# Kernel tuning notes

Measured on AMD Instinct MI355X. Metric: run time of the kernel, lower is better.

Reference implementation:

```python
import jax, jax.numpy as jnp
import numpy as np

S, E, K, D = 50000, 20000, 128, 128  # students, exercises, knowledge, emb dim
NE = 800000                          # edges per polarity
B = 8192                             # batch of response logs
L = 3                                # gcn layers
TEMP, CONTROL = 0.2, 0.3


def setup_inputs() -> dict:
    key = jax.random.key(0)
    ks = jax.random.split(key, 40)

    def nrm(i, shape, scale=0.05):
        return jax.random.normal(ks[i], shape, jnp.float32) * scale

    def uni(i, shape):
        return jax.random.uniform(ks[i], shape, jnp.float32)

    inp = {
        'stu_id': jax.random.randint(ks[0], (B,), 0, S, jnp.int32),
        'exer_id': jax.random.randint(ks[1], (B,), 0, E, jnp.int32),
        'kn_emb': uni(2, (B, K)),
        'ui1_u': jax.random.randint(ks[3], (NE,), 0, S, jnp.int32),
        'ui1_i': jax.random.randint(ks[4], (NE,), 0, E, jnp.int32),
        'ui1_val': uni(5, (NE,)), 'iu1_val': uni(6, (NE,)),
        'eps_ui1': uni(7, (NE,)), 'eps_iu1': uni(8, (NE,)),
        'ui0_u': jax.random.randint(ks[9], (NE,), 0, S, jnp.int32),
        'ui0_i': jax.random.randint(ks[10], (NE,), 0, E, jnp.int32),
        'ui0_val': uni(11, (NE,)), 'iu0_val': uni(12, (NE,)),
        'eps_ui0': uni(13, (NE,)), 'eps_iu0': uni(14, (NE,)),
        # embeddings
        'student_emb': nrm(15, (S, D)), 'exercise_emb': nrm(16, (E, D)),
        'knowledge_emb': nrm(17, (K, D)),
        'stu_b': nrm(18, (S, 1)), 'exer_b': nrm(19, (E, 1)), 'disc': nrm(20, (E, 1)),
        # edge-gate MLPs (polarity 1 and 0)
        'W1_l1': nrm(21, (D, 2 * D)), 'b1_l1': jnp.zeros((D,), jnp.float32),
        'W2_l1': nrm(22, (1, D)), 'b2_l1': jnp.zeros((1,), jnp.float32),
        'W1_l0': nrm(23, (D, 2 * D)), 'b1_l0': jnp.zeros((D,), jnp.float32),
        'W2_l0': nrm(24, (1, D)), 'b2_l0': jnp.zeros((1,), jnp.float32),
        # PosLinear prednet
        'pw1': nrm(25, (256, K)), 'pb1': jnp.zeros((256,), jnp.float32),
        'pw2': nrm(26, (128, 256)), 'pb2': jnp.zeros((128,), jnp.float32),
        'pw3': nrm(27, (1, 128)), 'pb3': jnp.zeros((1,), jnp.float32),
    }
    return inp


def _gate(uids, iids, uemb, iemb, W1, b1, W2, b2, eps):
    # concrete-distribution edge gate; embeddings are detached in original code
    row = jax.lax.stop_gradient(uemb)[uids]          # [NE, D]
    col = jax.lax.stop_gradient(iemb)[iids]          # [NE, D]
    h = jax.nn.relu(jnp.concatenate([row, col], axis=1) @ W1.T + b1)
    logit = (h @ W2.T + b2).reshape(-1)              # [NE]
    eps = jnp.clip(eps, 1e-6, 1.0 - 1e-6)
    g = jnp.log(eps) - jnp.log1p(-eps)               # logistic noise
    return CONTROL * jax.nn.sigmoid((logit + g) / TEMP) + (1.0 - CONTROL)


def _spmm(rows, cols, vals, x, n_rows):
    # out[rows] += vals * x[cols]
    return jax.ops.segment_sum(vals[:, None] * x[cols], rows, num_segments=n_rows)


def _poslin(x, W, b):
    Wp = 2.0 * jax.nn.relu(-W) + W  # == |W|
    return x @ Wp.T + b


def reference(stu_id, exer_id, kn_emb, ui1_u, ui1_i, ui1_val, iu1_val, eps_ui1,
              eps_iu1, ui0_u, ui0_i, ui0_val, iu0_val, eps_ui0, eps_iu0,
              student_emb, exercise_emb, knowledge_emb, stu_b, exer_b, disc,
              W1_l1, b1_l1, W2_l1, b2_l1, W1_l0, b1_l0, W2_l0, b2_l0,
              pw1, pb1, pw2, pb2, pw3, pb3):
    # --- graph_learner: per-edge gates on all 4 sparse matrices ---
    v_ui1 = ui1_val * _gate(ui1_u, ui1_i, student_emb, exercise_emb, W1_l1, b1_l1, W2_l1, b2_l1, eps_ui1)
    v_iu1 = iu1_val * _gate(ui1_u, ui1_i, student_emb, exercise_emb, W1_l1, b1_l1, W2_l1, b2_l1, eps_iu1)
    v_ui0 = ui0_val * _gate(ui0_u, ui0_i, student_emb, exercise_emb, W1_l0, b1_l0, W2_l0, b2_l0, eps_ui0)
    v_iu0 = iu0_val * _gate(ui0_u, ui0_i, student_emb, exercise_emb, W1_l0, b1_l0, W2_l0, b2_l0, eps_iu0)

    # --- graph_representations: L rounds of sparse propagation, mean over layers ---
    stu, exer = student_emb, exercise_emb
    stu_sum, exer_sum = stu, exer
    for _ in range(L):
        u1 = _spmm(ui1_u, ui1_i, v_ui1, exer, S)
        i1 = _spmm(ui1_i, ui1_u, v_iu1, stu, E)
        u0 = _spmm(ui0_u, ui0_i, v_ui0, exer, S)
        i0 = _spmm(ui0_i, ui0_u, v_iu0, stu, E)
        stu, exer = u1 + u0, i1 + i0
        stu_sum = stu_sum + stu
        exer_sum = exer_sum + exer
    stu_final = stu_sum / (L + 1)
    exer_final = exer_sum / (L + 1)

    # --- NCDM-style prediction head with PosLinear MLP ---
    stat = jax.nn.sigmoid(stu_final[stu_id] @ knowledge_emb.T + stu_b[stu_id])   # [B, K]
    diff = jax.nn.sigmoid(exer_final[exer_id] @ knowledge_emb.T + exer_b[exer_id])
    e_d = jax.nn.sigmoid(disc[exer_id])                                          # [B, 1]
    x = e_d * (stat - diff) * kn_emb
    h = jax.nn.sigmoid(_poslin(x, pw1, pb1))
    h = jax.nn.sigmoid(_poslin(h, pw2, pb2))
    out = jax.nn.sigmoid(_poslin(h, pw3, pb3)).reshape(-1)                       # [B]
    return out
```

## Files before the change

### kernel.cpp

```cpp
#include <hip/hip_runtime.h>
#include <hip/hip_bf16.h>
#include <math.h>

#define S_N 50000
#define E_N 20000
#define K_N 128
#define D_N 128
#define NE_N 800000
#define B_N 8192
#define L_N 3
#define GATE_TILES (NE_N / 64)
#define NB_S 782
#define NB_E 313
#define BPAD 464
#define BSLACK 480

typedef __attribute__((ext_vector_type(4))) float floatx4;
typedef __attribute__((ext_vector_type(8))) short short8v;

__device__ __forceinline__ unsigned short f2bf(float x) {
  unsigned int u = __float_as_uint(x);
  u += 0x7FFFu + ((u >> 16) & 1u);
  return (unsigned short)(u >> 16);
}
__device__ __forceinline__ float bf2f(unsigned short u) {
  return __uint_as_float(((unsigned int)u) << 16);
}
__device__ __forceinline__ float sigm(float z) { return 1.0f / (1.0f + __expf(-z)); }

__device__ __forceinline__ unsigned char f2e4m3(float x) {
  unsigned int u = __float_as_uint(x);
  unsigned char s = (unsigned char)((u >> 24) & 0x80);
  int e = (int)((u >> 23) & 0xFF) - 127;
  unsigned int m = u & 0x7FFFFF;
  if (((u >> 23) & 0xFF) == 0) return s;
  if (e >= 9) return s | 0x7E;
  if (e < -10) return s;
  if (e >= -6) {
    unsigned int keep = m >> 20;
    unsigned int rest = m & 0xFFFFF;
    if (rest > 0x80000u || (rest == 0x80000u && (keep & 1))) keep++;
    if (keep == 8) { keep = 0; e++; if (e >= 9) return s | 0x7E; }
    unsigned char b = (unsigned char)(s | ((e + 7) << 3) | keep);
    if ((b & 0x7F) == 0x7F) b = s | 0x7E;
    return b;
  }
  int shift = -6 - e;
  unsigned int full = 0x800000u | m;
  unsigned int q = full >> (20 + shift);
  unsigned int rest = full & ((1u << (20 + shift)) - 1);
  unsigned int half = 1u << (19 + shift);
  if (rest > half || (rest == half && (q & 1))) q++;
  if (q == 8) return s | 0x08;
  return (unsigned char)(s | q);
}
__device__ __forceinline__ unsigned int pk4_fp8(float4 v) {
  return (unsigned int)f2e4m3(v.x) | ((unsigned int)f2e4m3(v.y) << 8) |
         ((unsigned int)f2e4m3(v.z) << 16) | ((unsigned int)f2e4m3(v.w) << 24);
}

__global__ void prep_kernel(const float* __restrict__ W1_l1, const float* __restrict__ W1_l0,
                            const float* __restrict__ pw1, const float* __restrict__ pw2,
                            const float* __restrict__ pw3, const float* __restrict__ ke,
                            unsigned int* __restrict__ w1f8_1, unsigned int* __restrict__ w1f8_0,
                            float* __restrict__ pw1T, float* __restrict__ pw2T,
                            float* __restrict__ pw3a, float* __restrict__ keT) {
  int i = blockIdx.x * blockDim.x + threadIdx.x;
  if (i < 8192) { w1f8_1[i] = pk4_fp8(((const float4*)W1_l1)[i]); return; }
  i -= 8192;
  if (i < 8192) { w1f8_0[i] = pk4_fp8(((const float4*)W1_l0)[i]); return; }
  i -= 8192;
  if (i < 32768) { int d = i >> 8, j = i & 255; pw1T[i] = fabsf(pw1[j * 128 + d]); return; }
  i -= 32768;
  if (i < 32768) { int d = i >> 7, j = i & 127; pw2T[i] = fabsf(pw2[j * 256 + d]); return; }
  i -= 32768;
  if (i < 128) { pw3a[i] = fabsf(pw3[i]); return; }
  i -= 128;
  if (i < 16384) { int d = i >> 7, k = i & 127; keT[i] = ke[k * 128 + d]; return; }
}

__global__ void init_bf_kernel(const float* __restrict__ se, const float* __restrict__ ee,
                               unsigned short* __restrict__ sbf, unsigned short* __restrict__ ebf,
                               unsigned int* __restrict__ sf8, unsigned int* __restrict__ ef8) {
  int i = blockIdx.x * blockDim.x + threadIdx.x;
  const int nS4 = S_N * 32, nE4 = E_N * 32;
  if (i < nS4) {
    float4 v = ((const float4*)se)[i];
    unsigned int lo = (unsigned int)f2bf(v.x) | ((unsigned int)f2bf(v.y) << 16);
    unsigned int hi = (unsigned int)f2bf(v.z) | ((unsigned int)f2bf(v.w) << 16);
    ((uint2*)sbf)[i] = make_uint2(lo, hi);
    sf8[i] = pk4_fp8(v);
    return;
  }
  i -= nS4;
  if (i < nE4) {
    float4 v = ((const float4*)ee)[i];
    unsigned int lo = (unsigned int)f2bf(v.x) | ((unsigned int)f2bf(v.y) << 16);
    unsigned int hi = (unsigned int)f2bf(v.z) | ((unsigned int)f2bf(v.w) << 16);
    ((uint2*)ebf)[i] = make_uint2(lo, hi);
    ef8[i] = pk4_fp8(v);
  }
}

__global__ void zero_kernel(int* __restrict__ p, int n) {
  int i = blockIdx.x * blockDim.x + threadIdx.x;
  if (i < n) p[i] = 0;
}

__global__ __launch_bounds__(256)
void histB_kernel(const int* __restrict__ u1, const int* __restrict__ i1,
                  const int* __restrict__ u0, const int* __restrict__ i0,
                  int* __restrict__ gHistS, int* __restrict__ gHistE) {
  __shared__ int hS[NB_S], hE[NB_E];
  int t = threadIdx.x;
  for (int b = t; b < NB_S; b += 256) hS[b] = 0;
  for (int b = t; b < NB_E; b += 256) hE[b] = 0;
  __syncthreads();
  int e0 = blockIdx.x * 2048;
  for (int k = 0; k < 8; ++k) {
    int e = e0 + k * 256 + t;
    if (e < NE_N) {
      atomicAdd(&hS[u1[e] >> 6], 1);
      atomicAdd(&hS[u0[e] >> 6], 1);
      atomicAdd(&hE[i1[e] >> 6], 1);
      atomicAdd(&hE[i0[e] >> 6], 1);
    }
  }
  __syncthreads();
  for (int b = t; b < NB_S; b += 256) if (hS[b]) atomicAdd(&gHistS[b], hS[b]);
  for (int b = t; b < NB_E; b += 256) if (hE[b]) atomicAdd(&gHistE[b], hE[b]);
}

__global__ __launch_bounds__(128)
void scanB_kernel(const int* __restrict__ gHistS, int* __restrict__ baseS,
                  int* __restrict__ gCurS, int* __restrict__ basePS,
                  const int* __restrict__ gHistE, int* __restrict__ baseE,
                  int* __restrict__ gCurE, int* __restrict__ basePE) {
  int w = threadIdx.x >> 6, l = threadIdx.x & 63;
  int n = w ? NB_E : NB_S;
  const int* src = w ? gHistE : gHistS;
  int* bs  = w ? baseE  : baseS;
  int* cur = w ? gCurE  : gCurS;
  int* bsP = w ? basePE : basePS;
  int carry = 0, carryP = 0;
  for (int base = 0; base < n; base += 64) {
    int i = base + l;
    int v = (i < n) ? src[i] : 0;
    int p = (i < n) ? ((v + BPAD + 15) & ~15) : 0;
    int x = v, y = p;
#pragma unroll
    for (int o = 1; o < 64; o <<= 1) {
      int xx = __shfl_up(x, o, 64);
      int yy = __shfl_up(y, o, 64);
      if (l >= o) { x += xx; y += yy; }
    }
    if (i < n) {
      int ex = carry + x - v;
      bs[i] = ex; cur[i] = ex;
      bsP[i] = carryP + y - p;
    }
    carry += __shfl(x, 63, 64);
    carryP += __shfl(y, 63, 64);
  }
  if (l == 0) { bs[n] = carry; bsP[n] = carryP; }
}

__global__ __launch_bounds__(512, 2)
void gate_kernel(const int* __restrict__ eu1, const int* __restrict__ ei1,
                 const int* __restrict__ eu0, const int* __restrict__ ei0,
                 const unsigned char* __restrict__ sf8, const unsigned char* __restrict__ ef8,
                 const unsigned char* __restrict__ w1f8_1, const unsigned char* __restrict__ w1f8_0,
                 const float* __restrict__ b1_1, const float* __restrict__ w2_1,
                 const float* __restrict__ b2_1,
                 const float* __restrict__ b1_0, const float* __restrict__ w2_0,
                 const float* __restrict__ b2_0,
                 float* __restrict__ logit1, float* __restrict__ logit0) {
  __shared__ unsigned char Xl[2][64 * 272];
  __shared__ float plds[8][16];
  const int* eu; const int* ei; const unsigned char* w1f8;
  const float *b1p, *w2p, *b2p; float* lg;
  if (blockIdx.x < 2048) {
    eu = eu1; ei = ei1; w1f8 = w1f8_1; b1p = b1_1; w2p = w2_1; b2p = b2_1; lg = logit1;
  } else {
    eu = eu0; ei = ei0; w1f8 = w1f8_0; b1p = b1_0; w2p = w2_0; b2p = b2_0; lg = logit0;
  }
  int bb = blockIdx.x & 2047;
  int t = threadIdx.x;
  int wv = t >> 6, l = t & 63;
  int sub = l & 15, grp = l >> 4;
  int nh = wv & 1, rg = wv >> 1;
  int el = t >> 3, q = t & 7;

  long bfrag[4][8];
#pragma unroll
  for (int nt = 0; nt < 4; ++nt) {
    int col = nh * 64 + nt * 16 + sub;
#pragma unroll
    for (int ks = 0; ks < 8; ++ks)
      bfrag[nt][ks] = *(const long*)&w1f8[(col << 8) + ks * 32 + grp * 8];
  }
  float b1v[4], w2v[4];
#pragma unroll
  for (int nt = 0; nt < 4; ++nt) {
    int col = nh * 64 + nt * 16 + sub;
    b1v[nt] = b1p[col];
    w2v[nt] = w2p[col];
  }
  float b2s = b2p[0];

  uint4 c0, c1;
  {
    int eIdx = bb * 64 + el;
    const unsigned char* srcrow = (q < 4)
        ? sf8 + (size_t)eu[eIdx] * 128 + q * 32
        : ef8 + (size_t)ei[eIdx] * 128 + (q - 4) * 32;
    c0 = ((const uint4*)srcrow)[0];
    c1 = ((const uint4*)srcrow)[1];
    *(uint4*)&Xl[0][el * 272 + q * 32] = c0;
    *(uint4*)&Xl[0][el * 272 + q * 32 + 16] = c1;
  }
  int parity = 0;
  for (int tile = bb; tile < GATE_TILES; tile += 2048) {
    int nxt = tile + 2048;
    bool hasNext = (nxt < GATE_TILES);
    if (hasNext) {
      int eIdx = nxt * 64 + el;
      const unsigned char* srcrow = (q < 4)
          ? sf8 + (size_t)eu[eIdx] * 128 + q * 32
          : ef8 + (size_t)ei[eIdx] * 128 + (q - 4) * 32;
      c0 = ((const uint4*)srcrow)[0];
      c1 = ((const uint4*)srcrow)[1];
    }
    __syncthreads();

    floatx4 zero4 = {0.f, 0.f, 0.f, 0.f};
    floatx4 acc[4] = {zero4, zero4, zero4, zero4};
#pragma unroll
    for (int ks = 0; ks < 8; ++ks) {
      long a = *(const long*)&Xl[parity][(rg * 16 + sub) * 272 + ks * 32 + grp * 8];
#pragma unroll
      for (int nt = 0; nt < 4; ++nt)
        acc[nt] = __builtin_amdgcn_mfma_f32_16x16x32_fp8_fp8(a, bfrag[nt][ks], acc[nt], 0, 0, 0);
    }
    float p0 = 0, p1 = 0, p2 = 0, p3 = 0;
#pragma unroll
    for (int nt = 0; nt < 4; ++nt) {
      float bb2 = b1v[nt], ww = w2v[nt];
      p0 += fmaxf(acc[nt][0] + bb2, 0.0f) * ww;
      p1 += fmaxf(acc[nt][1] + bb2, 0.0f) * ww;
      p2 += fmaxf(acc[nt][2] + bb2, 0.0f) * ww;
      p3 += fmaxf(acc[nt][3] + bb2, 0.0f) * ww;
    }
#pragma unroll
    for (int m = 1; m < 16; m <<= 1) {
      p0 += __shfl_xor(p0, m, 64);
      p1 += __shfl_xor(p1, m, 64);
      p2 += __shfl_xor(p2, m, 64);
      p3 += __shfl_xor(p3, m, 64);
    }
    if (sub < 4) {
      float pv = (sub == 0) ? p0 : (sub == 1) ? p1 : (sub == 2) ? p2 : p3;
      plds[wv][grp * 4 + sub] = pv;
    }
    __syncthreads();
    if (wv == 0)
      lg[tile * 64 + l] = plds[(l >> 4) * 2][l & 15] + plds[(l >> 4) * 2 + 1][l & 15] + b2s;
    if (hasNext) {
      *(uint4*)&Xl[parity ^ 1][el * 272 + q * 32] = c0;
      *(uint4*)&Xl[parity ^ 1][el * 272 + q * 32 + 16] = c1;
    }
    parity ^= 1;
  }
}

__global__ __launch_bounds__(256)
void append_kernel(const int* __restrict__ u1, const int* __restrict__ i1,
                   const int* __restrict__ u0, const int* __restrict__ i0,
                   const float* __restrict__ logit1, const float* __restrict__ logit0,
                   const float* __restrict__ ui1_val, const float* __restrict__ iu1_val,
                   const float* __restrict__ eps_ui1, const float* __restrict__ eps_iu1,
                   const float* __restrict__ ui0_val, const float* __restrict__ iu0_val,
                   const float* __restrict__ eps_ui0, const float* __restrict__ eps_iu0,
                   int* __restrict__ gCurS, int* __restrict__ gCurE,
                   int2* __restrict__ recS, int2* __restrict__ recE) {
  __shared__ int hS[NB_S], hE[NB_E];
  int t = threadIdx.x;
  for (int b = t; b < NB_S; b += 256) hS[b] = 0;
  for (int b = t; b < NB_E; b += 256) hE[b] = 0;
  __syncthreads();
  int e0 = blockIdx.x * 2048;
  for (int k = 0; k < 8; ++k) {
    int e = e0 + k * 256 + t;
    if (e < NE_N) {
      atomicAdd(&hS[u1[e] >> 6], 1);
      atomicAdd(&hS[u0[e] >> 6], 1);
      atomicAdd(&hE[i1[e] >> 6], 1);
      atomicAdd(&hE[i0[e] >> 6], 1);
    }
  }
  __syncthreads();
  for (int b = t; b < NB_S; b += 256) { int c = hS[b]; hS[b] = c ? atomicAdd(&gCurS[b], c) : 0; }
  for (int b = t; b < NB_E; b += 256) { int c = hE[b]; hE[b] = c ? atomicAdd(&gCurE[b], c) : 0; }
  __syncthreads();
  for (int k = 0; k < 8; ++k) {
    int e = e0 + k * 256 + t;
    if (e < NE_N) {
      int a = u1[e], b = i1[e], c = u0[e], d = i0[e];
      float lg1 = logit1[e], lg0 = logit0[e];
      float ep, g, s2;
      ep = fminf(fmaxf(eps_ui1[e], 1e-6f), 1.0f - 1e-6f);
      g = __logf(ep) - log1pf(-ep);
      s2 = 1.0f / (1.0f + __expf(-(lg1 + g) * 5.0f));
      float v_ui1 = ui1_val[e] * (0.3f * s2 + 0.7f);
      ep = fminf(fmaxf(eps_iu1[e], 1e-6f), 1.0f - 1e-6f);
      g = __logf(ep) - log1pf(-ep);
      s2 = 1.0f / (1.0f + __expf(-(lg1 + g) * 5.0f));
      float v_iu1 = iu1_val[e] * (0.3f * s2 + 0.7f);
      ep = fminf(fmaxf(eps_ui0[e], 1e-6f), 1.0f - 1e-6f);
      g = __logf(ep) - log1pf(-ep);
      s2 = 1.0f / (1.0f + __expf(-(lg0 + g) * 5.0f));
      float v_ui0 = ui0_val[e] * (0.3f * s2 + 0.7f);
      ep = fminf(fmaxf(eps_iu0[e], 1e-6f), 1.0f - 1e-6f);
      g = __logf(ep) - log1pf(-ep);
      s2 = 1.0f / (1.0f + __expf(-(lg0 + g) * 5.0f));
      float v_iu0 = iu0_val[e] * (0.3f * s2 + 0.7f);
      int s;
      s = atomicAdd(&hS[a >> 6], 1); recS[s] = make_int2(((a & 63) << 16) | b, __float_as_int(v_ui1));
      s = atomicAdd(&hE[b >> 6], 1); recE[s] = make_int2(((b & 63) << 16) | a, __float_as_int(v_iu1));
      s = atomicAdd(&hS[c >> 6], 1); recS[s] = make_int2(((c & 63) << 16) | d, __float_as_int(v_ui0));
      s = atomicAdd(&hE[d >> 6], 1); recE[s] = make_int2(((d & 63) << 16) | c, __float_as_int(v_iu0));
    }
  }
}

__global__ __launch_bounds__(256)
void sortRow_kernel(const int* __restrict__ baseIn, const int* __restrict__ basePad,
                    const int2* __restrict__ rin_all, int2* __restrict__ rout_all,
                    int* __restrict__ rowPtr, int* __restrict__ rowCnt8, int nRowsTot) {
  __shared__ int cntR[64], offR[64], curR[64];
  int b = blockIdx.x, t = threadIdx.x;
  int bi = baseIn[b], cnt = baseIn[b + 1] - bi;
  int bo = basePad[b];
  int row0 = b * 64;
  const int2* rin = rin_all + bi;
  int2* rout = rout_all + bo;
  if (t < 64) cntR[t] = 0;
  __syncthreads();
  for (int j = t; j < cnt; j += 256) atomicAdd(&cntR[(rin[j].x >> 16) & 63], 1);
  __syncthreads();
  if (t < 64) {
    int p = (cntR[t] + 7) & ~7;
    int x = p;
#pragma unroll
    for (int o = 1; o < 64; o <<= 1) { int y = __shfl_up(x, o, 64); if (t >= o) x += y; }
    int ex = x - p;
    offR[t] = ex; curR[t] = ex;
    if (row0 + t < nRowsTot) {
      rowPtr[row0 + t] = bo + ex;
      rowCnt8[row0 + t] = p >> 3;
    }
  }
  __syncthreads();
  for (int j = t; j < cnt; j += 256) {
    int2 rc = rin[j];
    int r = (rc.x >> 16) & 63;
    int slot = atomicAdd(&curR[r], 1);
    rout[slot] = make_int2(rc.x & 0xFFFF, rc.y);
  }
  __syncthreads();
  if (t < 64) {
    int c = cntR[t], p = (c + 7) & ~7, o = offR[t];
    for (int j = c; j < p; ++j) rout[o + j] = make_int2(0, 0);
  }
}

__global__ __launch_bounds__(256)
void spmm_csr_kernel(const int* __restrict__ rowPtrS, const int* __restrict__ rowCnt8S,
                     const int2* __restrict__ rec2S,
                     const int* __restrict__ rowPtrE, const int* __restrict__ rowCnt8E,
                     const int2* __restrict__ rec2E,
                     const unsigned short* __restrict__ scur, const unsigned short* __restrict__ ecur,
                     unsigned short* __restrict__ snxt, unsigned short* __restrict__ enxt) {
  int gw = (blockIdx.x * 256 + threadIdx.x) >> 6;
  int l = threadIdx.x & 63;
  int g = l >> 3, lane8 = l & 7;
  if (gw >= S_N + E_N) return;
  const int2* rec; const unsigned short* src; unsigned short* dst;
  const int* rp; const int* rc8; int r;
  if (gw < S_N) { r = gw;       rp = rowPtrS; rc8 = rowCnt8S; rec = rec2S; src = ecur; dst = snxt; }
  else          { r = gw - S_N; rp = rowPtrE; rc8 = rowCnt8E; rec = rec2E; src = scur; dst = enxt; }
  int s0 = rp[r], n8 = rc8[r];
  float acc[16];
#pragma unroll
  for (int i = 0; i < 16; ++i) acc[i] = 0.f;
  for (int k = 0; k < n8; ++k) {
    int2 e = rec[s0 + k * 8 + g];
    float val = __int_as_float(e.y);
    const uint4* rowp = (const uint4*)(src + (size_t)e.x * 128);
    uint4 q0 = rowp[lane8 * 2];
    uint4 q1 = rowp[lane8 * 2 + 1];
#pragma unroll
    for (int i = 0; i < 4; ++i) {
      unsigned int w = ((const unsigned int*)&q0)[i];
      acc[2 * i]     = fmaf(val, bf2f((unsigned short)(w & 0xFFFF)), acc[2 * i]);
      acc[2 * i + 1] = fmaf(val, bf2f((unsigned short)(w >> 16)),    acc[2 * i + 1]);
    }
#pragma unroll
    for (int i = 0; i < 4; ++i) {
      unsigned int w = ((const unsigned int*)&q1)[i];
      acc[8 + 2 * i]     = fmaf(val, bf2f((unsigned short)(w & 0xFFFF)), acc[8 + 2 * i]);
      acc[8 + 2 * i + 1] = fmaf(val, bf2f((unsigned short)(w >> 16)),    acc[8 + 2 * i + 1]);
    }
  }
#pragma unroll
  for (int m = 8; m < 64; m <<= 1) {
#pragma unroll
    for (int i = 0; i < 16; ++i) acc[i] += __shfl_xor(acc[i], m, 64);
  }
  if (g == 0) {
    size_t base = (size_t)r * 128 + lane8 * 16;
    short8v o0, o1;
#pragma unroll
    for (int i = 0; i < 8; ++i) { o0[i] = (short)f2bf(acc[i]); o1[i] = (short)f2bf(acc[8 + i]); }
    *(short8v*)(dst + base) = o0;
    *(short8v*)(dst + base + 8) = o1;
  }
}

__global__ __launch_bounds__(256)
void head1_kernel(const int* __restrict__ stu_id, const int* __restrict__ exer_id,
                  const float* __restrict__ kn,
                  const unsigned short* __restrict__ sT0, const unsigned short* __restrict__ sT1,
                  const unsigned short* __restrict__ sT2, const unsigned short* __restrict__ sT3,
                  const unsigned short* __restrict__ eT0, const unsigned short* __restrict__ eT1,
                  const unsigned short* __restrict__ eT2, const unsigned short* __restrict__ eT3,
                  const float* __restrict__ keT,
                  const float* __restrict__ stub, const float* __restrict__ exeb,
                  const float* __restrict__ disc, float* __restrict__ xbuf) {
  __shared__ float srw[4][128], erw[4][128];
  int wv = threadIdx.x >> 6, l = threadIdx.x & 63;
  int b = blockIdx.x * 4 + wv;
  int sid = stu_id[b], eid = exer_id[b];
  size_t so = (size_t)sid * 128, eo = (size_t)eid * 128;
  float sx = 0.f, sy = 0.f, ex = 0.f, ey = 0.f;
  unsigned int w;
  w = ((const unsigned int*)(sT0 + so))[l]; sx += bf2f((unsigned short)(w & 0xFFFF)); sy += bf2f((unsigned short)(w >> 16));
  w = ((const unsigned int*)(sT1 + so))[l]; sx += bf2f((unsigned short)(w & 0xFFFF)); sy += bf2f((unsigned short)(w >> 16));
  w = ((const unsigned int*)(sT2 + so))[l]; sx += bf2f((unsigned short)(w & 0xFFFF)); sy += bf2f((unsigned short)(w >> 16));
  w = ((const unsigned int*)(sT3 + so))[l]; sx += bf2f((unsigned short)(w & 0xFFFF)); sy += bf2f((unsigned short)(w >> 16));
  w = ((const unsigned int*)(eT0 + eo))[l]; ex += bf2f((unsigned short)(w & 0xFFFF)); ey += bf2f((unsigned short)(w >> 16));
  w = ((const unsigned int*)(eT1 + eo))[l]; ex += bf2f((unsigned short)(w & 0xFFFF)); ey += bf2f((unsigned short)(w >> 16));
  w = ((const unsigned int*)(eT2 + eo))[l]; ex += bf2f((unsigned short)(w & 0xFFFF)); ey += bf2f((unsigned short)(w >> 16));
  w = ((const unsigned int*)(eT3 + eo))[l]; ex += bf2f((unsigned short)(w & 0xFFFF)); ey += bf2f((unsigned short)(w >> 16));
  srw[wv][2 * l] = sx * 0.25f; srw[wv][2 * l + 1] = sy * 0.25f;
  erw[wv][2 * l] = ex * 0.25f; erw[wv][2 * l + 1] = ey * 0.25f;
  __syncthreads();
  float s0 = 0, s1 = 0, d0 = 0, d1 = 0;
  for (int d = 0; d < 128; ++d) {
    float sd = srw[wv][d], ed = erw[wv][d];
    float ka = keT[d * 128 + l], kb = keT[d * 128 + l + 64];
    s0 = fmaf(sd, ka, s0); s1 = fmaf(sd, kb, s1);
    d0 = fmaf(ed, ka, d0); d1 = fmaf(ed, kb, d1);
  }
  float sbv = stub[sid], ebv = exeb[eid];
  float edv = sigm(disc[eid]);
  float st0 = sigm(s0 + sbv), st1 = sigm(s1 + sbv);
  float df0 = sigm(d0 + ebv), df1 = sigm(d1 + ebv);
  xbuf[(size_t)b * 128 + l]      = edv * (st0 - df0) * kn[(size_t)b * 128 + l];
  xbuf[(size_t)b * 128 + l + 64] = edv * (st1 - df1) * kn[(size_t)b * 128 + l + 64];
}

__global__ __launch_bounds__(256)
void head2_kernel(const float* __restrict__ xbuf, const float* __restrict__ pw1T,
                  const float* __restrict__ pb1, const float* __restrict__ pw2T,
                  const float* __restrict__ pb2, const float* __restrict__ pw3a,
                  const float* __restrict__ pb3, float* __restrict__ out) {
  __shared__ float xs[4][128], h1s[4][256], h2s[4][128];
  int wv = threadIdx.x >> 6, l = threadIdx.x & 63;
  int b = blockIdx.x * 4 + wv;
  xs[wv][l] = xbuf[(size_t)b * 128 + l];
  xs[wv][l + 64] = xbuf[(size_t)b * 128 + l + 64];
  __syncthreads();
#pragma unroll
  for (int q = 0; q < 4; ++q) {
    int j = q * 64 + l;
    float acc = 0.f;
    for (int d = 0; d < 128; ++d) acc = fmaf(xs[wv][d], pw1T[d * 256 + j], acc);
    h1s[wv][j] = sigm(acc + pb1[j]);
  }
  __syncthreads();
#pragma unroll
  for (int q = 0; q < 2; ++q) {
    int j = q * 64 + l;
    float acc = 0.f;
    for (int d = 0; d < 256; ++d) acc = fmaf(h1s[wv][d], pw2T[d * 128 + j], acc);
    h2s[wv][j] = sigm(acc + pb2[j]);
  }
  __syncthreads();
  float p = h2s[wv][l] * pw3a[l] + h2s[wv][l + 64] * pw3a[l + 64];
#pragma unroll
  for (int m = 1; m < 64; m <<= 1) p += __shfl_xor(p, m, 64);
  if (l == 0) out[b] = sigm(p + pb3[0]);
}

extern "C" void kernel_launch(void* const* d_in, const int* in_sizes, int n_in,
                              void* d_out, int out_size, void* d_ws, size_t ws_size,
                              hipStream_t stream) {
  const int*   stu_id  = (const int*)  d_in[0];
  const int*   exer_id = (const int*)  d_in[1];
  const float* kn_emb  = (const float*)d_in[2];
  const int*   ui1_u   = (const int*)  d_in[3];
  const int*   ui1_i   = (const int*)  d_in[4];
  const float* ui1_val = (const float*)d_in[5];
  const float* iu1_val = (const float*)d_in[6];
  const float* eps_ui1 = (const float*)d_in[7];
  const float* eps_iu1 = (const float*)d_in[8];
  const int*   ui0_u   = (const int*)  d_in[9];
  const int*   ui0_i   = (const int*)  d_in[10];
  const float* ui0_val = (const float*)d_in[11];
  const float* iu0_val = (const float*)d_in[12];
  const float* eps_ui0 = (const float*)d_in[13];
  const float* eps_iu0 = (const float*)d_in[14];
  const float* stu_emb = (const float*)d_in[15];
  const float* exe_emb = (const float*)d_in[16];
  const float* kno_emb = (const float*)d_in[17];
  const float* stu_b   = (const float*)d_in[18];
  const float* exe_b   = (const float*)d_in[19];
  const float* disc    = (const float*)d_in[20];
  const float* W1_l1   = (const float*)d_in[21];
  const float* b1_l1   = (const float*)d_in[22];
  const float* W2_l1   = (const float*)d_in[23];
  const float* b2_l1   = (const float*)d_in[24];
  const float* W1_l0   = (const float*)d_in[25];
  const float* b1_l0   = (const float*)d_in[26];
  const float* W2_l0   = (const float*)d_in[27];
  const float* b2_l0   = (const float*)d_in[28];
  const float* pw1     = (const float*)d_in[29];
  const float* pb1     = (const float*)d_in[30];
  const float* pw2     = (const float*)d_in[31];
  const float* pb2     = (const float*)d_in[32];
  const float* pw3     = (const float*)d_in[33];
  const float* pb3     = (const float*)d_in[34];
  float* out = (float*)d_out;
  (void)in_sizes; (void)n_in; (void)out_size; (void)ws_size;

  size_t off = 0;
  char* base = (char*)d_ws;
  auto carve = [&](size_t bytes) -> char* {
    char* p = base + off;
    off += (bytes + 255) & ~(size_t)255;
    return p;
  };
  unsigned int* w1f8_1 = (unsigned int*)carve(8192 * 4);
  unsigned int* w1f8_0 = (unsigned int*)carve(8192 * 4);
  float* pw1T = (float*)carve(32768 * 4);
  float* pw2T = (float*)carve(32768 * 4);
  float* pw3a = (float*)carve(128 * 4);
  float* keT  = (float*)carve(16384 * 4);
  char* vblock = carve((size_t)2 * NE_N * 8 + (size_t)BSLACK * NB_S * 8);
  unsigned short* stuT0 = (unsigned short*)carve((size_t)S_N * 128 * 2);
  unsigned short* stuT1 = (unsigned short*)carve((size_t)S_N * 128 * 2);
  unsigned short* stuT2 = (unsigned short*)carve((size_t)S_N * 128 * 2);
  unsigned short* stuT3 = (unsigned short*)carve((size_t)S_N * 128 * 2);
  unsigned short* exeT0 = (unsigned short*)carve((size_t)E_N * 128 * 2);
  unsigned short* exeT1 = (unsigned short*)carve((size_t)E_N * 128 * 2);
  unsigned short* exeT2 = (unsigned short*)carve((size_t)E_N * 128 * 2);
  unsigned short* exeT3 = (unsigned short*)carve((size_t)E_N * 128 * 2);
  unsigned int* sf8 = (unsigned int*)carve((size_t)S_N * 32 * 4);
  unsigned int* ef8 = (unsigned int*)carve((size_t)E_N * 32 * 4);
  float* logit1 = (float*)carve((size_t)NE_N * 4);
  float* logit0 = (float*)carve((size_t)NE_N * 4);
  int* gHistS = (int*)carve((size_t)(NB_S + NB_E) * 4);
  int* gHistE = gHistS + NB_S;
  int* baseSb  = (int*)carve((size_t)(NB_S + 1) * 4);
  int* baseEb  = (int*)carve((size_t)(NB_E + 1) * 4);
  int* basePSb = (int*)carve((size_t)(NB_S + 1) * 4);
  int* basePEb = (int*)carve((size_t)(NB_E + 1) * 4);
  int* gCurS  = (int*)carve((size_t)NB_S * 4);
  int* gCurE  = (int*)carve((size_t)NB_E * 4);
  int2* recS = (int2*)carve((size_t)2 * NE_N * 8 + (size_t)BSLACK * NB_E * 8);
  int2* recE = (int2*)carve((size_t)2 * NE_N * 8);
  int* rowPtrS  = (int*)carve((size_t)S_N * 4);
  int* rowCnt8S = (int*)carve((size_t)S_N * 4);
  int* rowPtrE  = (int*)carve((size_t)E_N * 4);
  int* rowCnt8E = (int*)carve((size_t)E_N * 4);
  float* xbuf = (float*)carve((size_t)B_N * 128 * 4);
  int2* rec2S = (int2*)vblock;
  int2* rec2E = recS;

  prep_kernel<<<(98432 + 255) / 256, 256, 0, stream>>>(W1_l1, W1_l0, pw1, pw2, pw3, kno_emb,
                                                       w1f8_1, w1f8_0, pw1T, pw2T, pw3a, keT);
  init_bf_kernel<<<(2240000 + 255) / 256, 256, 0, stream>>>(stu_emb, exe_emb, stuT0, exeT0,
                                                            sf8, ef8);
  zero_kernel<<<(NB_S + NB_E + 255) / 256, 256, 0, stream>>>(gHistS, NB_S + NB_E);
  histB_kernel<<<(NE_N + 2047) / 2048, 256, 0, stream>>>(ui1_u, ui1_i, ui0_u, ui0_i,
                                                         gHistS, gHistE);
  scanB_kernel<<<1, 128, 0, stream>>>(gHistS, baseSb, gCurS, basePSb,
                                      gHistE, baseEb, gCurE, basePEb);
  gate_kernel<<<4096, 512, 0, stream>>>(ui1_u, ui1_i, ui0_u, ui0_i,
                                        (const unsigned char*)sf8, (const unsigned char*)ef8,
                                        (const unsigned char*)w1f8_1, (const unsigned char*)w1f8_0,
                                        b1_l1, W2_l1, b2_l1, b1_l0, W2_l0, b2_l0,
                                        logit1, logit0);
  append_kernel<<<(NE_N + 2047) / 2048, 256, 0, stream>>>(ui1_u, ui1_i, ui0_u, ui0_i,
                                                          logit1, logit0,
                                                          ui1_val, iu1_val, eps_ui1, eps_iu1,
                                                          ui0_val, iu0_val, eps_ui0, eps_iu0,
                                                          gCurS, gCurE, recS, recE);
  sortRow_kernel<<<NB_S, 256, 0, stream>>>(baseSb, basePSb, recS, rec2S,
                                           rowPtrS, rowCnt8S, S_N);
  sortRow_kernel<<<NB_E, 256, 0, stream>>>(baseEb, basePEb, recE, rec2E,
                                           rowPtrE, rowCnt8E, E_N);
  unsigned short* stuT[4] = {stuT0, stuT1, stuT2, stuT3};
  unsigned short* exeT[4] = {exeT0, exeT1, exeT2, exeT3};
  for (int layer = 0; layer < L_N; ++layer) {
    spmm_csr_kernel<<<(S_N + E_N + 3) / 4, 256, 0, stream>>>(
        rowPtrS, rowCnt8S, rec2S, rowPtrE, rowCnt8E, rec2E,
        stuT[layer], exeT[layer], stuT[layer + 1], exeT[layer + 1]);
  }
  head1_kernel<<<B_N / 4, 256, 0, stream>>>(stu_id, exer_id, kn_emb,
                                            stuT0, stuT1, stuT2, stuT3,
                                            exeT0, exeT1, exeT2, exeT3,
                                            keT, stu_b, exe_b, disc, xbuf);
  head2_kernel<<<B_N / 4, 256, 0, stream>>>(xbuf, pw1T, pb1, pw2T, pb2, pw3a, pb3, out);
}
```

Baseline: 660.0 us.

## Pack CSR records into 32-bit and presort each bucket by column

Each edge record is compressed from an int2 into one 32-bit word holding a 16-bit column index and a bf16 edge value. This halves the index traffic read by the spmm loop. A new sortCol pass orders each row bucket by column range before the row sort, so gathers within a row touch nearby source rows and get better cache locality. The cost is an extra sort kernel per polarity plus bf16 rounding of the edge weights.

```diff
diff --git a/kernel.cpp b/kernel.cpp
--- a/kernel.cpp
+++ b/kernel.cpp
@@ -334,8 +334,42 @@
 }
 
 __global__ __launch_bounds__(256)
+void sortCol_kernel(const int* __restrict__ baseIn, const int2* __restrict__ rin_all,
+                    int2* __restrict__ rout_all) {
+  __shared__ int cnt2[128], incl[128], cur2[128];
+  int b = blockIdx.x, t = threadIdx.x;
+  int bi = baseIn[b], cnt = baseIn[b + 1] - bi;
+  const int2* rin = rin_all + bi;
+  int2* rout = rout_all + bi;
+  if (t < 128) cnt2[t] = 0;
+  __syncthreads();
+  for (int j = t; j < cnt; j += 256) atomicAdd(&cnt2[(rin[j].x & 0xFFFF) >> 9], 1);
+  __syncthreads();
+  if (t < 128) {
+    int l = t & 63;
+    int v = cnt2[t];
+    int x = v;
+#pragma unroll
+    for (int o = 1; o < 64; o <<= 1) { int y = __shfl_up(x, o, 64); if (l >= o) x += y; }
+    incl[t] = x;
+  }
+  __syncthreads();
+  if (t < 128) {
+    int ex = incl[t] - cnt2[t];
+    if (t >= 64) ex += incl[63];
+    cur2[t] = ex;
+  }
+  __syncthreads();
+  for (int j = t; j < cnt; j += 256) {
+    int2 rc = rin[j];
+    int slot = atomicAdd(&cur2[(rc.x & 0xFFFF) >> 9], 1);
+    rout[slot] = rc;
+  }
+}
+
+__global__ __launch_bounds__(256)
 void sortRow_kernel(const int* __restrict__ baseIn, const int* __restrict__ basePad,
-                    const int2* __restrict__ rin_all, int2* __restrict__ rout_all,
+                    const int2* __restrict__ rin_all, int* __restrict__ rout_all,
                     int* __restrict__ rowPtr, int* __restrict__ rowCnt8, int nRowsTot) {
   __shared__ int cntR[64], offR[64], curR[64];
   int b = blockIdx.x, t = threadIdx.x;
@@ -343,7 +377,7 @@
   int bo = basePad[b];
   int row0 = b * 64;
   const int2* rin = rin_all + bi;
-  int2* rout = rout_all + bo;
+  int* rout = rout_all + bo;
   if (t < 64) cntR[t] = 0;
   __syncthreads();
   for (int j = t; j < cnt; j += 256) atomicAdd(&cntR[(rin[j].x >> 16) & 63], 1);
@@ -365,38 +399,38 @@
     int2 rc = rin[j];
     int r = (rc.x >> 16) & 63;
     int slot = atomicAdd(&curR[r], 1);
-    rout[slot] = make_int2(rc.x & 0xFFFF, rc.y);
+    rout[slot] = (rc.x & 0xFFFF) | ((int)f2bf(__int_as_float(rc.y)) << 16);
   }
   __syncthreads();
   if (t < 64) {
     int c = cntR[t], p = (c + 7) & ~7, o = offR[t];
-    for (int j = c; j < p; ++j) rout[o + j] = make_int2(0, 0);
+    for (int j = c; j < p; ++j) rout[o + j] = 0;
   }
 }
 
 __global__ __launch_bounds__(256)
 void spmm_csr_kernel(const int* __restrict__ rowPtrS, const int* __restrict__ rowCnt8S,
-                     const int2* __restrict__ rec2S,
+                     const int* __restrict__ rec4S,
                      const int* __restrict__ rowPtrE, const int* __restrict__ rowCnt8E,
-                     const int2* __restrict__ rec2E,
+                     const int* __restrict__ rec4E,
                      const unsigned short* __restrict__ scur, const unsigned short* __restrict__ ecur,
                      unsigned short* __restrict__ snxt, unsigned short* __restrict__ enxt) {
   int gw = (blockIdx.x * 256 + threadIdx.x) >> 6;
   int l = threadIdx.x & 63;
   int g = l >> 3, lane8 = l & 7;
   if (gw >= S_N + E_N) return;
-  const int2* rec; const unsigned short* src; unsigned short* dst;
+  const int* rec; const unsigned short* src; unsigned short* dst;
   const int* rp; const int* rc8; int r;
-  if (gw < S_N) { r = gw;       rp = rowPtrS; rc8 = rowCnt8S; rec = rec2S; src = ecur; dst = snxt; }
-  else          { r = gw - S_N; rp = rowPtrE; rc8 = rowCnt8E; rec = rec2E; src = scur; dst = enxt; }
+  if (gw < S_N) { r = gw;       rp = rowPtrS; rc8 = rowCnt8S; rec = rec4S; src = ecur; dst = snxt; }
+  else          { r = gw - S_N; rp = rowPtrE; rc8 = rowCnt8E; rec = rec4E; src = scur; dst = enxt; }
   int s0 = rp[r], n8 = rc8[r];
   float acc[16];
 #pragma unroll
   for (int i = 0; i < 16; ++i) acc[i] = 0.f;
   for (int k = 0; k < n8; ++k) {
-    int2 e = rec[s0 + k * 8 + g];
-    float val = __int_as_float(e.y);
-    const uint4* rowp = (const uint4*)(src + (size_t)e.x * 128);
+    int e = rec[s0 + k * 8 + g];
+    float val = bf2f((unsigned short)(e >> 16));
+    const uint4* rowp = (const uint4*)(src + (size_t)(e & 0xFFFF) * 128);
     uint4 q0 = rowp[lane8 * 2];
     uint4 q1 = rowp[lane8 * 2 + 1];
 #pragma unroll
@@ -585,8 +619,9 @@
   int* rowPtrE  = (int*)carve((size_t)E_N * 4);
   int* rowCnt8E = (int*)carve((size_t)E_N * 4);
   float* xbuf = (float*)carve((size_t)B_N * 128 * 4);
-  int2* rec2S = (int2*)vblock;
-  int2* rec2E = recS;
+  int2* tmpRec = (int2*)sf8;
+  int*  rec4S  = (int*)vblock;
+  int*  rec4E  = (int*)recS;
 
   prep_kernel<<<(98432 + 255) / 256, 256, 0, stream>>>(W1_l1, W1_l0, pw1, pw2, pw3, kno_emb,
                                                        w1f8_1, w1f8_0, pw1T, pw2T, pw3a, keT);
@@ -607,15 +642,17 @@
                                                           ui1_val, iu1_val, eps_ui1, eps_iu1,
                                                           ui0_val, iu0_val, eps_ui0, eps_iu0,
                                                           gCurS, gCurE, recS, recE);
-  sortRow_kernel<<<NB_S, 256, 0, stream>>>(baseSb, basePSb, recS, rec2S,
+  sortCol_kernel<<<NB_S, 256, 0, stream>>>(baseSb, recS, tmpRec);
+  sortRow_kernel<<<NB_S, 256, 0, stream>>>(baseSb, basePSb, tmpRec, rec4S,
                                            rowPtrS, rowCnt8S, S_N);
-  sortRow_kernel<<<NB_E, 256, 0, stream>>>(baseEb, basePEb, recE, rec2E,
+  sortCol_kernel<<<NB_E, 256, 0, stream>>>(baseEb, recE, tmpRec);
+  sortRow_kernel<<<NB_E, 256, 0, stream>>>(baseEb, basePEb, tmpRec, rec4E,
                                            rowPtrE, rowCnt8E, E_N);
   unsigned short* stuT[4] = {stuT0, stuT1, stuT2, stuT3};
   unsigned short* exeT[4] = {exeT0, exeT1, exeT2, exeT3};
   for (int layer = 0; layer < L_N; ++layer) {
     spmm_csr_kernel<<<(S_N + E_N + 3) / 4, 256, 0, stream>>>(
-        rowPtrS, rowCnt8S, rec2S, rowPtrE, rowCnt8E, rec2E,
+        rowPtrS, rowCnt8S, rec4S, rowPtrE, rowCnt8E, rec4E,
         stuT[layer], exeT[layer], stuT[layer + 1], exeT[layer + 1]);
   }
   head1_kernel<<<B_N / 4, 256, 0, stream>>>(stu_id, exer_id, kn_emb,
```

After: 674.5 us. 2.2% more time.
